# Optimization experiments

Hardware: AMD Instinct MI355X
Metric: run time of the kernel (lower is better)

## Reference

```python
import jax, jax.numpy as jnp
import numpy as np

# (vocab_size, offset, length) per feature id; alternating single/multi-valued
FEATURE_SPECS = [(100000, 0, 1), (100000, 1, 20), (100000, 21, 1), (100000, 22, 20),
                 (100000, 42, 1), (100000, 43, 20), (100000, 63, 1), (100000, 64, 20),
                 (100000, 84, 1), (100000, 85, 20), (100000, 105, 1), (100000, 106, 20),
                 (100000, 126, 1), (100000, 127, 20), (100000, 147, 1), (100000, 148, 20)]
GROUPS = [[0, 1, 2, 3], [4, 5, 6, 7], [8, 9, 10, 11], [12, 13, 14, 15]]
B, NF, V, E, D, G = 4096, 16, 100001, 64, 512, 4
TOTAL_INT_DIM = 168
LN_EPS = 1e-5


def setup_inputs() -> dict:
    key = jax.random.key(0)
    k0, k1, k2, k3 = jax.random.split(key, 4)
    int_feats = jax.random.randint(k0, (B, TOTAL_INT_DIM), 0, V, dtype=jnp.int32)
    emb_tables = jax.random.normal(k1, (NF, V, E), dtype=jnp.float32) * 0.02
    W = jax.random.normal(k2, (G, len(GROUPS[0]) * E, D), dtype=jnp.float32) * 0.02
    b = jnp.zeros((G, D), dtype=jnp.float32)
    gamma = jnp.ones((G, D), dtype=jnp.float32)
    beta = jnp.zeros((G, D), dtype=jnp.float32)
    return {"int_feats": int_feats, "emb_tables": emb_tables, "W": W, "b": b,
            "gamma": gamma, "beta": beta}


def _forward(int_feats, emb_tables, W, b, gamma, beta):
    # padding_idx=0 -> row 0 is zero (also makes grads to row 0 vanish)
    tables = emb_tables.at[:, 0, :].set(0.0)
    fid_embs = []
    for i, (vs, off, length) in enumerate(FEATURE_SPECS):
        if length == 1:
            e = tables[i][int_feats[:, off]]                       # (B, E)
        else:
            vals = int_feats[:, off:off + length]                  # (B, L)
            emb = tables[i][vals]                                  # (B, L, E)
            mask = (vals != 0).astype(emb.dtype)[..., None]        # (B, L, 1)
            cnt = jnp.clip(mask.sum(axis=1), 1.0)                  # (B, 1)
            e = (emb * mask).sum(axis=1) / cnt                     # (B, E)
        fid_embs.append(e)
    tokens = []
    for g, grp in enumerate(GROUPS):
        cat = jnp.concatenate([fid_embs[j] for j in grp], axis=-1)  # (B, 4*E)
        h = cat @ W[g] + b[g]                                       # (B, D)
        mu = h.mean(axis=-1, keepdims=True)
        var = ((h - mu) ** 2).mean(axis=-1, keepdims=True)          # biased, as torch LN
        hn = (h - mu) / jnp.sqrt(var + LN_EPS) * gamma[g] + beta[g]
        tokens.append(jax.nn.silu(hn))
    return jnp.stack(tokens, axis=1)                                # (B, G, D)


def reference(int_feats, emb_tables, W, b, gamma, beta):
    return _forward(int_feats, emb_tables, W, b, gamma, beta)
```

## Files before the change

kernel.cpp:

```cpp
#include <hip/hip_runtime.h>
#include <hip/hip_bf16.h>

typedef __attribute__((ext_vector_type(8))) short short8;
typedef __attribute__((ext_vector_type(4))) float f32x4;

#define V_TAB 100001
#define B_N   4096

__global__ __launch_bounds__(256) void pool_kernel(
    const int* __restrict__ feats,
    const float* __restrict__ tables,
    __hip_bfloat16* __restrict__ pooled)
{
    const int b    = blockIdx.x;
    const int wave = threadIdx.x >> 6;
    const int lane = threadIdx.x & 63;
    const int* fr  = feats + b * 168;

    #pragma unroll
    for (int k = 0; k < 4; ++k) {
        const int f   = wave * 4 + k;
        const int off = (f >> 1) * 21 + (f & 1);
        const float* tab = tables + (size_t)f * (V_TAB * 64);
        float acc;
        if ((f & 1) == 0) {
            const int idx = fr[off];
            const float v = tab[idx * 64 + lane];
            acc = (idx != 0) ? v : 0.f;
        } else {
            int idxv = (lane < 20) ? fr[off + lane] : 0;
            int   idxs[20];
            float vals[20];
            #pragma unroll
            for (int j = 0; j < 20; ++j) {
                idxs[j] = __shfl(idxv, j);
                vals[j] = tab[idxs[j] * 64 + lane];
            }
            acc = 0.f; int cnt = 0;
            #pragma unroll
            for (int j = 0; j < 20; ++j) {
                if (idxs[j] != 0) { acc += vals[j]; cnt++; }
            }
            acc *= 1.f / (float)(cnt > 0 ? cnt : 1);
        }
        pooled[(b * 16 + f) * 64 + lane] = __float2bfloat16(acc);
    }
}

__global__ __launch_bounds__(256) void wprep_kernel(
    const float* __restrict__ W,
    __hip_bfloat16* __restrict__ Wsw)
{
    const int idx = blockIdx.x * 256 + threadIdx.x;
    int rem = idx;
    const int j    = rem & 7;   rem >>= 3;
    const int lane = rem & 63;  rem >>= 6;
    const int ks   = rem & 7;   rem >>= 3;
    const int nt   = rem & 7;   rem >>= 3;
    const int w    = rem & 3;   rem >>= 2;
    const int g    = rem;
    const int n = w * 128 + nt * 16 + (lane & 15);
    const int kk = ks * 32 + (lane >> 4) * 8 + j;
    Wsw[idx] = __float2bfloat16(W[(g * 256 + kk) * 512 + n]);
}

__global__ __launch_bounds__(256) void gemm_ln_silu(
    const __hip_bfloat16* __restrict__ pooled,
    const __hip_bfloat16* __restrict__ Wsw,
    const float* __restrict__ bias,
    const float* __restrict__ gamma,
    const float* __restrict__ beta,
    float* __restrict__ out)
{
    const int g       = blockIdx.y;
    const int rowbase = blockIdx.x * 32;
    const int wave = threadIdx.x >> 6;
    const int lane = threadIdx.x & 63;
    const int l15  = lane & 15;
    const int lg   = lane >> 4;
    const int wcol = wave * 128;

    f32x4 acc[2][8];
    #pragma unroll
    for (int mt = 0; mt < 2; ++mt)
        #pragma unroll
        for (int nt = 0; nt < 8; ++nt) acc[mt][nt] = (f32x4){0.f, 0.f, 0.f, 0.f};

    const short* wbase = (const short*)Wsw + (((size_t)(g * 4 + wave) * 64) * 64 + lane) * 8;
    const short* abase = (const short*)pooled + (size_t)(rowbase + l15) * 1024 + g * 256 + lg * 8;

    #pragma unroll
    for (int ks = 0; ks < 8; ++ks) {
        const short8 a0 = *(const short8*)(abase + ks * 32);
        const short8 a1 = *(const short8*)(abase + 16 * 1024 + ks * 32);
        #pragma unroll
        for (int nt = 0; nt < 8; ++nt) {
            const short8 bf = *(const short8*)(wbase + (size_t)(nt * 8 + ks) * 64 * 8);
            acc[0][nt] = __builtin_amdgcn_mfma_f32_16x16x32_bf16(a0, bf, acc[0][nt], 0, 0, 0);
            acc[1][nt] = __builtin_amdgcn_mfma_f32_16x16x32_bf16(a1, bf, acc[1][nt], 0, 0, 0);
        }
    }

    float gv[8], tv[8];
    #pragma unroll
    for (int nt = 0; nt < 8; ++nt) {
        const int col = wcol + nt * 16 + l15;
        const float bv = bias[g * 512 + col];
        gv[nt] = gamma[g * 512 + col];
        tv[nt] = beta[g * 512 + col];
        #pragma unroll
        for (int r = 0; r < 4; ++r) { acc[0][nt][r] += bv; acc[1][nt][r] += bv; }
    }

    __shared__ float red[32][4][2];
    #pragma unroll
    for (int mt = 0; mt < 2; ++mt)
        #pragma unroll
        for (int r = 0; r < 4; ++r) {
            float s = 0.f, q = 0.f;
            #pragma unroll
            for (int nt = 0; nt < 8; ++nt) { const float v = acc[mt][nt][r]; s += v; q += v * v; }
            #pragma unroll
            for (int m = 1; m < 16; m <<= 1) { s += __shfl_xor(s, m); q += __shfl_xor(q, m); }
            if (l15 == 0) {
                const int row = mt * 16 + lg * 4 + r;
                red[row][wave][0] = s;
                red[row][wave][1] = q;
            }
        }
    __syncthreads();

    __shared__ float mu_s[32], ri_s[32];
    if (threadIdx.x < 32) {
        const int row = threadIdx.x;
        const float s = red[row][0][0] + red[row][1][0] + red[row][2][0] + red[row][3][0];
        const float q = red[row][0][1] + red[row][1][1] + red[row][2][1] + red[row][3][1];
        const float mu  = s * (1.f / 512.f);
        const float var = q * (1.f / 512.f) - mu * mu;
        mu_s[row] = mu;
        ri_s[row] = rsqrtf(var + 1e-5f);
    }
    __syncthreads();

    #pragma unroll
    for (int mt = 0; mt < 2; ++mt)
        #pragma unroll
        for (int r = 0; r < 4; ++r) {
            const int row = mt * 16 + lg * 4 + r;
            const float mu = mu_s[row];
            const float ri = ri_s[row];
            float* orow = out + ((size_t)(rowbase + row) * 4 + g) * 512 + wcol;
            #pragma unroll
            for (int nt = 0; nt < 8; ++nt) {
                const float h  = acc[mt][nt][r];
                const float hn = (h - mu) * ri * gv[nt] + tv[nt];
                orow[nt * 16 + l15] = hn / (1.f + __expf(-hn));
            }
        }
}

extern "C" void kernel_launch(void* const* d_in, const int* in_sizes, int n_in,
                              void* d_out, int out_size, void* d_ws, size_t ws_size,
                              hipStream_t stream) {
    const int*   feats  = (const int*)d_in[0];
    const float* tables = (const float*)d_in[1];
    const float* W      = (const float*)d_in[2];
    const float* bias   = (const float*)d_in[3];
    const float* gamma  = (const float*)d_in[4];
    const float* beta   = (const float*)d_in[5];
    float* out = (float*)d_out;

    __hip_bfloat16* pooled = (__hip_bfloat16*)d_ws;
    __hip_bfloat16* Wsw    = (__hip_bfloat16*)((char*)d_ws + (size_t)B_N * 16 * 64 * 2);

    pool_kernel<<<dim3(B_N), dim3(256), 0, stream>>>(feats, tables, pooled);
    wprep_kernel<<<dim3(2048), dim3(256), 0, stream>>>(W, Wsw);
    gemm_ln_silu<<<dim3(128, 4), dim3(256), 0, stream>>>(pooled, Wsw, bias, gamma, beta, out);
}
```

Measured before the change: 514.4 us.

## Restructure pooling per feature pair, coalesce W prep, stage A in LDS with B prefetch

The pooling kernel now launches twice as many blocks, and each wave handles one single/multi feature pair. It issues all 20 gathers plus the single lookup at once, which raises memory-level parallelism for the random table reads. The weight-prep kernel now reads W coalesced and scatters its writes. The GEMM stages its A tile in LDS, double-buffers the B fragments in registers across k-steps, and asks for 2 blocks per CU. This adds register pressure and an LDS barrier.

```diff
diff --git a/kernel.cpp b/kernel.cpp
--- a/kernel.cpp
+++ b/kernel.cpp
@@ -13,38 +13,31 @@
     __hip_bfloat16* __restrict__ pooled)
 {
     const int b    = blockIdx.x;
-    const int wave = threadIdx.x >> 6;
+    const int p    = blockIdx.y * 4 + (threadIdx.x >> 6);
     const int lane = threadIdx.x & 63;
-    const int* fr  = feats + b * 168;
+    const int* fr  = feats + b * 168 + p * 21;
+    const float* tab_s = tables + (size_t)(2 * p) * (V_TAB * 64);
+    const float* tab_m = tab_s + (size_t)(V_TAB * 64);
 
+    const int idx_s = fr[0];
+    const float v_s = tab_s[(size_t)idx_s * 64 + lane];
+
+    int   idxs[20];
+    float vals[20];
     #pragma unroll
-    for (int k = 0; k < 4; ++k) {
-        const int f   = wave * 4 + k;
-        const int off = (f >> 1) * 21 + (f & 1);
-        const float* tab = tables + (size_t)f * (V_TAB * 64);
-        float acc;
-        if ((f & 1) == 0) {
-            const int idx = fr[off];
-            const float v = tab[idx * 64 + lane];
-            acc = (idx != 0) ? v : 0.f;
-        } else {
-            int idxv = (lane < 20) ? fr[off + lane] : 0;
-            int   idxs[20];
-            float vals[20];
-            #pragma unroll
-            for (int j = 0; j < 20; ++j) {
-                idxs[j] = __shfl(idxv, j);
-                vals[j] = tab[idxs[j] * 64 + lane];
-            }
-            acc = 0.f; int cnt = 0;
-            #pragma unroll
-            for (int j = 0; j < 20; ++j) {
-                if (idxs[j] != 0) { acc += vals[j]; cnt++; }
-            }
-            acc *= 1.f / (float)(cnt > 0 ? cnt : 1);
-        }
-        pooled[(b * 16 + f) * 64 + lane] = __float2bfloat16(acc);
-    }
+    for (int j = 0; j < 20; ++j) idxs[j] = fr[1 + j];
+    #pragma unroll
+    for (int j = 0; j < 20; ++j) vals[j] = tab_m[(size_t)idxs[j] * 64 + lane];
+
+    float acc = 0.f; int cnt = 0;
+    #pragma unroll
+    for (int j = 0; j < 20; ++j)
+        if (idxs[j] != 0) { acc += vals[j]; ++cnt; }
+    acc *= 1.f / (float)(cnt > 0 ? cnt : 1);
+
+    __hip_bfloat16* orow = pooled + ((size_t)b * 16 + 2 * p) * 64;
+    orow[lane]      = __float2bfloat16((idx_s != 0) ? v_s : 0.f);
+    orow[64 + lane] = __float2bfloat16(acc);
 }
 
 __global__ __launch_bounds__(256) void wprep_kernel(
@@ -52,19 +45,21 @@
     __hip_bfloat16* __restrict__ Wsw)
 {
     const int idx = blockIdx.x * 256 + threadIdx.x;
-    int rem = idx;
-    const int j    = rem & 7;   rem >>= 3;
-    const int lane = rem & 63;  rem >>= 6;
-    const int ks   = rem & 7;   rem >>= 3;
-    const int nt   = rem & 7;   rem >>= 3;
-    const int w    = rem & 3;   rem >>= 2;
-    const int g    = rem;
-    const int n = w * 128 + nt * 16 + (lane & 15);
-    const int kk = ks * 32 + (lane >> 4) * 8 + j;
-    Wsw[idx] = __float2bfloat16(W[(g * 256 + kk) * 512 + n]);
+    const int n   = idx & 511;
+    const int kk  = (idx >> 9) & 255;
+    const int g   = idx >> 17;
+    const int w   = n >> 7;
+    const int nt  = (n >> 4) & 7;
+    const int l15 = n & 15;
+    const int ks  = kk >> 5;
+    const int lg  = (kk >> 3) & 3;
+    const int j   = kk & 7;
+    const int lane = lg * 16 + l15;
+    const int dst = ((((g * 4 + w) * 8 + nt) * 8 + ks) * 64 + lane) * 8 + j;
+    Wsw[dst] = __float2bfloat16(W[idx]);
 }
 
-__global__ __launch_bounds__(256) void gemm_ln_silu(
+__global__ __launch_bounds__(256, 2) void gemm_ln_silu(
     const __hip_bfloat16* __restrict__ pooled,
     const __hip_bfloat16* __restrict__ Wsw,
     const float* __restrict__ bias,
@@ -80,25 +75,48 @@
     const int lg   = lane >> 4;
     const int wcol = wave * 128;
 
+    __shared__ short lds_a[32 * 264];
+    {
+        const int r  = threadIdx.x >> 3;
+        const int c0 = threadIdx.x & 7;
+        const short* src = (const short*)pooled + (size_t)(rowbase + r) * 1024 + g * 256;
+        #pragma unroll
+        for (int i = 0; i < 4; ++i) {
+            const int c = c0 + i * 8;
+            *(short8*)(lds_a + r * 264 + c * 8) = *(const short8*)(src + c * 8);
+        }
+    }
+    __syncthreads();
+
     f32x4 acc[2][8];
     #pragma unroll
     for (int mt = 0; mt < 2; ++mt)
         #pragma unroll
         for (int nt = 0; nt < 8; ++nt) acc[mt][nt] = (f32x4){0.f, 0.f, 0.f, 0.f};
 
-    const short* wbase = (const short*)Wsw + (((size_t)(g * 4 + wave) * 64) * 64 + lane) * 8;
-    const short* abase = (const short*)pooled + (size_t)(rowbase + l15) * 1024 + g * 256 + lg * 8;
+    const short* wptr = (const short*)Wsw + ((size_t)(g * 4 + wave) * 4096 + lane) * 8;
 
+    short8 bcur[8], bnxt[8];
     #pragma unroll
+    for (int nt = 0; nt < 8; ++nt)
+        bcur[nt] = *(const short8*)(wptr + (size_t)(nt * 8) * 512);
+
+    #pragma unroll 1
     for (int ks = 0; ks < 8; ++ks) {
-        const short8 a0 = *(const short8*)(abase + ks * 32);
-        const short8 a1 = *(const short8*)(abase + 16 * 1024 + ks * 32);
+        if (ks < 7) {
+            #pragma unroll
+            for (int nt = 0; nt < 8; ++nt)
+                bnxt[nt] = *(const short8*)(wptr + (size_t)(nt * 8 + ks + 1) * 512);
+        }
+        const short8 a0 = *(const short8*)(lds_a + l15 * 264 + ks * 32 + lg * 8);
+        const short8 a1 = *(const short8*)(lds_a + (16 + l15) * 264 + ks * 32 + lg * 8);
         #pragma unroll
         for (int nt = 0; nt < 8; ++nt) {
-            const short8 bf = *(const short8*)(wbase + (size_t)(nt * 8 + ks) * 64 * 8);
-            acc[0][nt] = __builtin_amdgcn_mfma_f32_16x16x32_bf16(a0, bf, acc[0][nt], 0, 0, 0);
-            acc[1][nt] = __builtin_amdgcn_mfma_f32_16x16x32_bf16(a1, bf, acc[1][nt], 0, 0, 0);
+            acc[0][nt] = __builtin_amdgcn_mfma_f32_16x16x32_bf16(a0, bcur[nt], acc[0][nt], 0, 0, 0);
+            acc[1][nt] = __builtin_amdgcn_mfma_f32_16x16x32_bf16(a1, bcur[nt], acc[1][nt], 0, 0, 0);
         }
+        #pragma unroll
+        for (int nt = 0; nt < 8; ++nt) bcur[nt] = bnxt[nt];
     }
 
     float gv[8], tv[8];
@@ -173,7 +191,7 @@
     __hip_bfloat16* pooled = (__hip_bfloat16*)d_ws;
     __hip_bfloat16* Wsw    = (__hip_bfloat16*)((char*)d_ws + (size_t)B_N * 16 * 64 * 2);
 
-    pool_kernel<<<dim3(B_N), dim3(256), 0, stream>>>(feats, tables, pooled);
+    pool_kernel<<<dim3(B_N, 2), dim3(256), 0, stream>>>(feats, tables, pooled);
     wprep_kernel<<<dim3(2048), dim3(256), 0, stream>>>(W, Wsw);
     gemm_ln_silu<<<dim3(128, 4), dim3(256), 0, stream>>>(pooled, Wsw, bias, gamma, beta, out);
 }
```

After: 505.4 us. No clear change (-1.7%).
